# Kernel tuning notes

Hardware: AMD Instinct MI355X
Metric: run time of the kernel (lower is better)

The kernel has to match this reference:

```python
import jax, jax.numpy as jnp
import numpy as np
from jax import lax

DILATIONS = [1, 2, 4, 8, 16, 32, 64, 128, 256, 512] * 2  # 20 layers
C = 128   # residual channels
K = 2     # kernel size


def _causal_dilated_conv(x, w, b, d):
    # x: [B, C, T], w: [2C, C, K], left-pad by d*(K-1) for causality
    pad = d * (K - 1)
    y = lax.conv_general_dilated(
        x, w, window_strides=(1,), padding=[(pad, 0)],
        rhs_dilation=(d,), dimension_numbers=('NCH', 'OIH', 'NCH'))
    return y + b[None, :, None]


def setup_inputs() -> dict:
    key = jax.random.key(0)
    ks = jax.random.split(key, 5)
    L = len(DILATIONS)
    x = jax.random.normal(ks[0], (4, C, 8192), jnp.float32)
    # 0.05 scale keeps activations stable through 20 residual layers
    w_conv = jax.random.normal(ks[1], (L, 2 * C, C, K), jnp.float32) * 0.05
    b_conv = jax.random.normal(ks[2], (L, 2 * C), jnp.float32) * 0.05
    w_out = jax.random.normal(ks[3], (L, C, C), jnp.float32) * 0.05
    b_out = jax.random.normal(ks[4], (L, C), jnp.float32) * 0.05
    return {"x": x, "w_conv": w_conv, "b_conv": b_conv,
            "w_out": w_out, "b_out": b_out}


def reference(x, w_conv, b_conv, w_out, b_out):
    """WaveNet convolution stack: per layer, causal dilated conv -> gated
    tanh*sigmoid -> 1x1 output conv; residual add; collect skips.
    Returns (output [B,C,T], skips [L,B,C,T])."""
    skips = []
    for i, d in enumerate(DILATIONS):
        h = x
        z = _causal_dilated_conv(x, w_conv[i], b_conv[i], d)  # [B, 2C, T]
        g = jnp.tanh(z[:, :C]) * jax.nn.sigmoid(z[:, C:])      # gated, [B, C, T]
        s = jnp.einsum('oc,bct->bot', w_out[i], g) + b_out[i][None, :, None]
        x = s + h  # residual connection
        skips.append(s)
    return x, jnp.stack(skips)
```

## Files before the change

### kernel.cpp

```cpp
#include <hip/hip_runtime.h>
#include <hip/hip_bf16.h>
#include <stdint.h>

using f32x4  = __attribute__((ext_vector_type(4))) float;
using bf16x8 = __attribute__((ext_vector_type(8))) short;
using bf16x4 = __attribute__((ext_vector_type(4))) short;

#define NB   4
#define NC   128
#define NT   8192
#define TL   64
#define NLAYER 20
#define GROWB 272
#define CONVN (NLAYER * 256 * 256)
#define WOUTN (NLAYER * 128 * 128)
#define PACKB ((CONVN + WOUTN + 255) / 256)
#define TRANB ((NT / 64) * (NC / 64) * NB)

__device__ __forceinline__ short f2b(float f) {
  union { float f; unsigned u; } v; v.f = f;
  unsigned r = v.u + 0x7FFFu + ((v.u >> 16) & 1u);
  return (short)(r >> 16);
}

__device__ __forceinline__ float b2f(short s) {
  union { unsigned u; float f; } v;
  v.u = ((unsigned)(unsigned short)s) << 16;
  return v.f;
}

__device__ __forceinline__ f32x4 mfma16(bf16x8 a, bf16x8 b, f32x4 c) {
  return __builtin_amdgcn_mfma_f32_16x16x32_bf16(a, b, c, 0, 0, 0);
}

__device__ __forceinline__ void gl_lds16(const void* g, void* l) {
  __builtin_amdgcn_global_load_lds(
      (const __attribute__((address_space(1))) void*)g,
      (__attribute__((address_space(3))) void*)l, 16, 0, 0);
}

__global__ void prep(const float* __restrict__ x,
                     const float* __restrict__ w_conv,
                     const float* __restrict__ w_out,
                     short* __restrict__ xtb,
                     short* __restrict__ wcb, short* __restrict__ wob) {
  __shared__ float tile[64][65];
  if (blockIdx.x < PACKB) {
    const int idx = blockIdx.x * 256 + threadIdx.x;
    if (idx < CONVN) {
      const int k = idx & 255, o = (idx >> 8) & 255, lyr = idx >> 16;
      const int tap = k >> 7, c = k & 127;
      wcb[idx] = f2b(w_conv[(((size_t)lyr * 256 + o) * 128 + c) * 2 + tap]);
    } else if (idx < CONVN + WOUTN) {
      const int j = idx - CONVN;
      wob[j] = f2b(w_out[j]);
    }
    return;
  }
  const int bid2 = blockIdx.x - PACKB;
  const int t0 = (bid2 & 127) * 64;
  const int c0 = ((bid2 >> 7) & 1) * 64;
  const int b  = bid2 >> 8;
  const int lane = threadIdx.x & 63;
  const int r4   = threadIdx.x >> 6;
  #pragma unroll
  for (int i = 0; i < 16; ++i) {
    const int cl = i * 4 + r4;
    tile[cl][lane] = x[((size_t)(b * NC + c0 + cl)) * NT + t0 + lane];
  }
  __syncthreads();
  #pragma unroll
  for (int it = 0; it < 2; ++it) {
    const int idx = it * 256 + threadIdx.x;
    const int r  = idx >> 3;
    const int gi = idx & 7;
    bf16x8 v;
    #pragma unroll
    for (int jj = 0; jj < 8; ++jj) v[jj] = f2b(tile[gi * 8 + jj][r]);
    const int t = t0 + r;
    const int ci = ((c0 >> 3) + gi) ^ (t & 7);
    *(bf16x8*)((char*)xtb + ((size_t)(b * NT + t)) * 256 + ci * 16) = v;
  }
}

__global__ __launch_bounds__(512, 4)
void wavenet_pair(const short* __restrict__ wcb,
                  const float* __restrict__ b_conv,
                  const short* __restrict__ wob,
                  const float* __restrict__ b_out,
                  const short* __restrict__ xbin,
                  short* __restrict__ xbout,
                  float* __restrict__ out,
                  int L, int d1, int d2)
{
  __shared__ char ldsY[80 * 256];
  __shared__ char ldsXG[88 * 256 + 80 * 256];
  char* X = ldsXG;
  char* G = ldsXG + 88 * 256;
  char* S = ldsXG;

  const int tid = threadIdx.x;
  const int w = tid >> 6, l = tid & 63, lh = l & 15, lq = l >> 4;
  const int o0 = 16 * w + lq * 4;
  const int uid = (blockIdx.x & 7) * 64 + (blockIdx.x >> 3);
  const int b   = uid >> 7;
  const int t0  = (uid & 127) * 64;
  const bool zhalo = (t0 == 0);
  const f32x4 fz = {0.f, 0.f, 0.f, 0.f};
  const size_t XOFFS = (size_t)NB * NC * NT;

  if (!zhalo) {
    const char* src = (const char*)xbin + ((size_t)(b * NT + t0 - 24)) * 256;
    #pragma unroll
    for (int k = 0; k < 3; ++k) {
      const int off = k * 8192 + tid * 16;
      if (off < 88 * 256) gl_lds16(src + off, X + off);
    }
  } else {
    if (tid * 16 < 6144) {
      bf16x8 z = {0, 0, 0, 0, 0, 0, 0, 0};
      *(bf16x8*)(X + tid * 16) = z;
    }
    const char* src = (const char*)xbin + ((size_t)(b * NT)) * 256;
    gl_lds16(src + tid * 16,        X + 6144 + tid * 16);
    gl_lds16(src + tid * 16 + 8192, X + 6144 + tid * 16 + 8192);
  }
  __syncthreads();

  f32x4 acc1[2][5];
  #pragma unroll
  for (int mi = 0; mi < 2; ++mi)
    #pragma unroll
    for (int nn = 0; nn < 5; ++nn) acc1[mi][nn] = fz;
  {
    const short* wl = wcb + (size_t)L * 65536;
    #pragma unroll
    for (int ks = 0; ks < 8; ++ks) {
      const bf16x8 a0 = *(const bf16x8*)(wl + (16 * w + lh) * 256 + ks * 32 + lq * 8);
      const bf16x8 a1 = *(const bf16x8*)(wl + (128 + 16 * w + lh) * 256 + ks * 32 + lq * 8);
      const int dd = (ks < 4) ? d1 : 0;
      #pragma unroll
      for (int nn = 0; nn < 5; ++nn) {
        const int p = 8 + nn * 16 + lh - dd;
        const int ci = ((ks & 3) * 4 + lq) ^ (p & 7);
        const bf16x8 bb = *(const bf16x8*)(X + p * 256 + ci * 16);
        acc1[0][nn] = mfma16(a0, bb, acc1[0][nn]);
        acc1[1][nn] = mfma16(a1, bb, acc1[1][nn]);
      }
    }
  }
  {
    float ba[4], bs[4];
    #pragma unroll
    for (int r = 0; r < 4; ++r) {
      ba[r] = b_conv[L * 256 + o0 + r];
      bs[r] = b_conv[L * 256 + 128 + o0 + r];
    }
    #pragma unroll
    for (int nn = 0; nn < 5; ++nn) {
      bf16x4 g4;
      #pragma unroll
      for (int r = 0; r < 4; ++r) {
        const float za = acc1[0][nn][r] + ba[r];
        const float zb = acc1[1][nn][r] + bs[r];
        const float th = 1.f - 2.f / (1.f + __expf(2.f * za));
        const float sg = 1.f / (1.f + __expf(-zb));
        g4[r] = f2b(th * sg);
      }
      const int q = nn * 16 + lh;
      const int ci = (o0 >> 3) ^ (q & 7);
      *(bf16x4*)(G + q * 256 + ci * 16 + (o0 & 7) * 2) = g4;
    }
  }
  __syncthreads();

  f32x4 s4vL[4];
  {
    f32x4 acc2[5];
    #pragma unroll
    for (int nn = 0; nn < 5; ++nn) acc2[nn] = fz;
    const short* wol = wob + (size_t)L * 16384;
    #pragma unroll
    for (int ks = 0; ks < 4; ++ks) {
      const bf16x8 a = *(const bf16x8*)(wol + (16 * w + lh) * 128 + ks * 32 + lq * 8);
      #pragma unroll
      for (int nn = 0; nn < 5; ++nn) {
        const int q = nn * 16 + lh;
        const int ci = (ks * 4 + lq) ^ (q & 7);
        const bf16x8 bb = *(const bf16x8*)(G + q * 256 + ci * 16);
        acc2[nn] = mfma16(a, bb, acc2[nn]);
      }
    }
    float bo[4];
    #pragma unroll
    for (int r = 0; r < 4; ++r) bo[r] = b_out[L * 128 + o0 + r];
    #pragma unroll
    for (int nn = 0; nn < 5; ++nn) {
      const int q = nn * 16 + lh;
      const int p = q + 8;
      const int ci = (o0 >> 3) ^ (q & 7);
      const bf16x4 h4 = *(const bf16x4*)(X + p * 256 + ci * 16 + (o0 & 7) * 2);
      f32x4 s4, xn;
      #pragma unroll
      for (int r = 0; r < 4; ++r) {
        s4[r] = acc2[nn][r] + bo[r];
        xn[r] = s4[r] + b2f(h4[r]);
      }
      if (nn >= 1) s4vL[nn - 1] = s4;
      bf16x4 x4;
      #pragma unroll
      for (int r = 0; r < 4; ++r) x4[r] = f2b(xn[r]);
      if (zhalo && nn == 0) { x4[0] = 0; x4[1] = 0; x4[2] = 0; x4[3] = 0; }
      *(bf16x4*)(ldsY + q * 256 + ci * 16 + (o0 & 7) * 2) = x4;
    }
  }
  __syncthreads();

  #pragma unroll
  for (int nn = 0; nn < 4; ++nn) {
    const int tt = nn * 16 + lh;
    #pragma unroll
    for (int r = 0; r < 4; ++r) {
      const int o  = o0 + r;
      const int lg = tt >> 2;
      const int pg = (lg & 8) | ((lg ^ (o & 7)) & 7);
      *(float*)(S + o * 256 + pg * 16 + (tt & 3) * 4) = s4vL[nn][r];
    }
  }
  __syncthreads();

  f32x4 acc1b[2][4];
  #pragma unroll
  for (int mi = 0; mi < 2; ++mi)
    #pragma unroll
    for (int n = 0; n < 4; ++n) acc1b[mi][n] = fz;
  {
    float* skipBase = out + XOFFS + ((size_t)((L * NB + b) * NC)) * NT + t0;
    const int j8 = tid & 7;
    #pragma unroll
    for (int half = 0; half < 2; ++half) {
      const int o = half * 64 + (tid >> 3);
      #pragma unroll
      for (int k = 0; k < 2; ++k) {
        const int pg = (k * 8) | ((j8 ^ (o & 7)) & 7);
        const f32x4 v = *(const f32x4*)(S + o * 256 + pg * 16);
        __builtin_nontemporal_store(v, (f32x4*)(skipBase + (size_t)o * NT + j8 * 4 + k * 32));
      }
    }
    const short* wl2 = wcb + (size_t)(L + 1) * 65536;
    #pragma unroll
    for (int ks = 0; ks < 8; ++ks) {
      const bf16x8 a0 = *(const bf16x8*)(wl2 + (16 * w + lh) * 256 + ks * 32 + lq * 8);
      const bf16x8 a1 = *(const bf16x8*)(wl2 + (128 + 16 * w + lh) * 256 + ks * 32 + lq * 8);
      const int dd = (ks < 4) ? d2 : 0;
      #pragma unroll
      for (int n = 0; n < 4; ++n) {
        const int qy = 16 + n * 16 + lh - dd;
        const int ci = ((ks & 3) * 4 + lq) ^ (qy & 7);
        const bf16x8 bb = *(const bf16x8*)(ldsY + qy * 256 + ci * 16);
        acc1b[0][n] = mfma16(a0, bb, acc1b[0][n]);
        acc1b[1][n] = mfma16(a1, bb, acc1b[1][n]);
      }
    }
  }
  __syncthreads();

  {
    float ba[4], bs[4];
    #pragma unroll
    for (int r = 0; r < 4; ++r) {
      ba[r] = b_conv[(L + 1) * 256 + o0 + r];
      bs[r] = b_conv[(L + 1) * 256 + 128 + o0 + r];
    }
    #pragma unroll
    for (int n = 0; n < 4; ++n) {
      bf16x4 g4;
      #pragma unroll
      for (int r = 0; r < 4; ++r) {
        const float za = acc1b[0][n][r] + ba[r];
        const float zb = acc1b[1][n][r] + bs[r];
        const float th = 1.f - 2.f / (1.f + __expf(2.f * za));
        const float sg = 1.f / (1.f + __expf(-zb));
        g4[r] = f2b(th * sg);
      }
      const int q2 = n * 16 + lh;
      const int ci = (o0 >> 3) ^ (q2 & 7);
      *(bf16x4*)(G + q2 * 256 + ci * 16 + (o0 & 7) * 2) = g4;
    }
  }
  __syncthreads();

  f32x4 s4vP[4];
  {
    f32x4 acc2[4];
    #pragma unroll
    for (int n = 0; n < 4; ++n) acc2[n] = fz;
    const short* wol2 = wob + (size_t)(L + 1) * 16384;
    #pragma unroll
    for (int ks = 0; ks < 4; ++ks) {
      const bf16x8 a = *(const bf16x8*)(wol2 + (16 * w + lh) * 128 + ks * 32 + lq * 8);
      #pragma unroll
      for (int n = 0; n < 4; ++n) {
        const int q2 = n * 16 + lh;
        const int ci = (ks * 4 + lq) ^ (q2 & 7);
        const bf16x8 bb = *(const bf16x8*)(G + q2 * 256 + ci * 16);
        acc2[n] = mfma16(a, bb, acc2[n]);
      }
    }
    float bo[4];
    #pragma unroll
    for (int r = 0; r < 4; ++r) bo[r] = b_out[(L + 1) * 128 + o0 + r];
    #pragma unroll
    for (int n = 0; n < 4; ++n) {
      const int q = 16 + n * 16 + lh;
      const int ci = (o0 >> 3) ^ (q & 7);
      const bf16x4 h4 = *(const bf16x4*)(ldsY + q * 256 + ci * 16 + (o0 & 7) * 2);
      f32x4 s4, xn;
      #pragma unroll
      for (int r = 0; r < 4; ++r) {
        s4[r] = acc2[n][r] + bo[r];
        xn[r] = s4[r] + b2f(h4[r]);
      }
      s4vP[n] = s4;
      bf16x4 x4;
      #pragma unroll
      for (int r = 0; r < 4; ++r) x4[r] = f2b(xn[r]);
      *(bf16x4*)(ldsY + q * 256 + ci * 16 + (o0 & 7) * 2) = x4;
    }
  }
  __syncthreads();

  #pragma unroll
  for (int n = 0; n < 4; ++n) {
    const int tt = n * 16 + lh;
    #pragma unroll
    for (int r = 0; r < 4; ++r) {
      const int o  = o0 + r;
      const int lg = tt >> 2;
      const int pg = (lg & 8) | ((lg ^ (o & 7)) & 7);
      *(float*)(S + o * 256 + pg * 16 + (tt & 3) * 4) = s4vP[n][r];
    }
  }
  __syncthreads();

  {
    float* skipBase = out + XOFFS + ((size_t)(((L + 1) * NB + b) * NC)) * NT + t0;
    const int j8 = tid & 7;
    #pragma unroll
    for (int half = 0; half < 2; ++half) {
      const int o = half * 64 + (tid >> 3);
      #pragma unroll
      for (int k = 0; k < 2; ++k) {
        const int pg = (k * 8) | ((j8 ^ (o & 7)) & 7);
        const f32x4 v = *(const f32x4*)(S + o * 256 + pg * 16);
        __builtin_nontemporal_store(v, (f32x4*)(skipBase + (size_t)o * NT + j8 * 4 + k * 32));
      }
    }
    char* dstBase = (char*)xbout + ((size_t)(b * NT + t0)) * 256;
    #pragma unroll
    for (int k = 0; k < 2; ++k) {
      const int idx = k * 512 + tid;
      const int r = idx >> 4, pcol = idx & 15;
      *(f32x4*)(dstBase + r * 256 + pcol * 16) =
          *(const f32x4*)(ldsY + (16 + r) * 256 + pcol * 16);
    }
  }
}

__global__ __launch_bounds__(512, 4)
void wavenet_pair6(const short* __restrict__ wcb,
                   const float* __restrict__ b_conv,
                   const short* __restrict__ wob,
                   const float* __restrict__ b_out,
                   const short* __restrict__ xbin,
                   short* __restrict__ xbout,
                   float* __restrict__ out,
                   int L, int d1, int d2)
{
  __shared__ char ldsY[96 * 256];
  __shared__ char ldsXG[112 * 256 + 96 * 256];
  char* X = ldsXG;
  char* G = ldsXG + 112 * 256;
  char* S = ldsXG;

  const int tid = threadIdx.x;
  const int w = tid >> 6, l = tid & 63, lh = l & 15, lq = l >> 4;
  const int o0 = 16 * w + lq * 4;
  const int uid = (blockIdx.x & 7) * 64 + (blockIdx.x >> 3);
  const int b   = uid >> 7;
  const int t0  = (uid & 127) * 64;
  const bool zhalo = (t0 == 0);
  const f32x4 fz = {0.f, 0.f, 0.f, 0.f};
  const size_t XOFFS = (size_t)NB * NC * NT;

  if (!zhalo) {
    const char* src = (const char*)xbin + ((size_t)(b * NT + t0 - 48)) * 256;
    #pragma unroll
    for (int k = 0; k < 4; ++k) {
      const int off = k * 8192 + tid * 16;
      if (off < 112 * 256) gl_lds16(src + off, X + off);
    }
  } else {
    if (tid * 16 < 12288) {
      bf16x8 z = {0, 0, 0, 0, 0, 0, 0, 0};
      *(bf16x8*)(X + tid * 16) = z;
      if (tid * 16 + 8192 < 12288) *(bf16x8*)(X + tid * 16 + 8192) = z;
    }
    const char* src = (const char*)xbin + ((size_t)(b * NT)) * 256;
    gl_lds16(src + tid * 16,        X + 12288 + tid * 16);
    gl_lds16(src + tid * 16 + 8192, X + 12288 + tid * 16 + 8192);
  }
  __syncthreads();

  f32x4 acc1[2][6];
  #pragma unroll
  for (int mi = 0; mi < 2; ++mi)
    #pragma unroll
    for (int nn = 0; nn < 6; ++nn) acc1[mi][nn] = fz;
  {
    const short* wl = wcb + (size_t)L * 65536;
    #pragma unroll
    for (int ks = 0; ks < 8; ++ks) {
      const bf16x8 a0 = *(const bf16x8*)(wl + (16 * w + lh) * 256 + ks * 32 + lq * 8);
      const bf16x8 a1 = *(const bf16x8*)(wl + (128 + 16 * w + lh) * 256 + ks * 32 + lq * 8);
      const int dd = (ks < 4) ? d1 : 0;
      #pragma unroll
      for (int nn = 0; nn < 6; ++nn) {
        const int p = 16 + nn * 16 + lh - dd;
        const int ci = ((ks & 3) * 4 + lq) ^ (p & 7);
        const bf16x8 bb = *(const bf16x8*)(X + p * 256 + ci * 16);
        acc1[0][nn] = mfma16(a0, bb, acc1[0][nn]);
        acc1[1][nn] = mfma16(a1, bb, acc1[1][nn]);
      }
    }
  }
  {
    float ba[4], bs[4];
    #pragma unroll
    for (int r = 0; r < 4; ++r) {
      ba[r] = b_conv[L * 256 + o0 + r];
      bs[r] = b_conv[L * 256 + 128 + o0 + r];
    }
    #pragma unroll
    for (int nn = 0; nn < 6; ++nn) {
      bf16x4 g4;
      #pragma unroll
      for (int r = 0; r < 4; ++r) {
        const float za = acc1[0][nn][r] + ba[r];
        const float zb = acc1[1][nn][r] + bs[r];
        const float th = 1.f - 2.f / (1.f + __expf(2.f * za));
        const float sg = 1.f / (1.f + __expf(-zb));
        g4[r] = f2b(th * sg);
      }
      const int q = nn * 16 + lh;
      const int ci = (o0 >> 3) ^ (q & 7);
      *(bf16x4*)(G + q * 256 + ci * 16 + (o0 & 7) * 2) = g4;
    }
  }
  __syncthreads();

  f32x4 s4vL[4];
  {
    f32x4 acc2[6];
    #pragma unroll
    for (int nn = 0; nn < 6; ++nn) acc2[nn] = fz;
    const short* wol = wob + (size_t)L * 16384;
    #pragma unroll
    for (int ks = 0; ks < 4; ++ks) {
      const bf16x8 a = *(const bf16x8*)(wol + (16 * w + lh) * 128 + ks * 32 + lq * 8);
      #pragma unroll
      for (int nn = 0; nn < 6; ++nn) {
        const int q = nn * 16 + lh;
        const int ci = (ks * 4 + lq) ^ (q & 7);
        const bf16x8 bb = *(const bf16x8*)(G + q * 256 + ci * 16);
        acc2[nn] = mfma16(a, bb, acc2[nn]);
      }
    }
    float bo[4];
    #pragma unroll
    for (int r = 0; r < 4; ++r) bo[r] = b_out[L * 128 + o0 + r];
    #pragma unroll
    for (int nn = 0; nn < 6; ++nn) {
      const int q = nn * 16 + lh;
      const int p = q + 16;
      const int ci = (o0 >> 3) ^ (q & 7);
      const bf16x4 h4 = *(const bf16x4*)(X + p * 256 + ci * 16 + (o0 & 7) * 2);
      f32x4 s4, xn;
      #pragma unroll
      for (int r = 0; r < 4; ++r) {
        s4[r] = acc2[nn][r] + bo[r];
        xn[r] = s4[r] + b2f(h4[r]);
      }
      if (nn >= 2) s4vL[nn - 2] = s4;
      bf16x4 x4;
      #pragma unroll
      for (int r = 0; r < 4; ++r) x4[r] = f2b(xn[r]);
      if (zhalo && nn < 2) { x4[0] = 0; x4[1] = 0; x4[2] = 0; x4[3] = 0; }
      *(bf16x4*)(ldsY + q * 256 + ci * 16 + (o0 & 7) * 2) = x4;
    }
  }
  __syncthreads();

  #pragma unroll
  for (int nn = 0; nn < 4; ++nn) {
    const int tt = nn * 16 + lh;
    #pragma unroll
    for (int r = 0; r < 4; ++r) {
      const int o  = o0 + r;
      const int lg = tt >> 2;
      const int pg = (lg & 8) | ((lg ^ (o & 7)) & 7);
      *(float*)(S + o * 256 + pg * 16 + (tt & 3) * 4) = s4vL[nn][r];
    }
  }
  __syncthreads();

  f32x4 acc1b[2][4];
  #pragma unroll
  for (int mi = 0; mi < 2; ++mi)
    #pragma unroll
    for (int n = 0; n < 4; ++n) acc1b[mi][n] = fz;
  {
    float* skipBase = out + XOFFS + ((size_t)((L * NB + b) * NC)) * NT + t0;
    const int j8 = tid & 7;
    #pragma unroll
    for (int half = 0; half < 2; ++half) {
      const int o = half * 64 + (tid >> 3);
      #pragma unroll
      for (int k = 0; k < 2; ++k) {
        const int pg = (k * 8) | ((j8 ^ (o & 7)) & 7);
        const f32x4 v = *(const f32x4*)(S + o * 256 + pg * 16);
        __builtin_nontemporal_store(v, (f32x4*)(skipBase + (size_t)o * NT + j8 * 4 + k * 32));
      }
    }
    const short* wl2 = wcb + (size_t)(L + 1) * 65536;
    #pragma unroll
    for (int ks = 0; ks < 8; ++ks) {
      const bf16x8 a0 = *(const bf16x8*)(wl2 + (16 * w + lh) * 256 + ks * 32 + lq * 8);
      const bf16x8 a1 = *(const bf16x8*)(wl2 + (128 + 16 * w + lh) * 256 + ks * 32 + lq * 8);
      const int dd = (ks < 4) ? d2 : 0;
      #pragma unroll
      for (int n = 0; n < 4; ++n) {
        const int qy = 32 + n * 16 + lh - dd;
        const int ci = ((ks & 3) * 4 + lq) ^ (qy & 7);
        const bf16x8 bb = *(const bf16x8*)(ldsY + qy * 256 + ci * 16);
        acc1b[0][n] = mfma16(a0, bb, acc1b[0][n]);
        acc1b[1][n] = mfma16(a1, bb, acc1b[1][n]);
      }
    }
  }
  __syncthreads();

  {
    float ba[4], bs[4];
    #pragma unroll
    for (int r = 0; r < 4; ++r) {
      ba[r] = b_conv[(L + 1) * 256 + o0 + r];
      bs[r] = b_conv[(L + 1) * 256 + 128 + o0 + r];
    }
    #pragma unroll
    for (int n = 0; n < 4; ++n) {
      bf16x4 g4;
      #pragma unroll
      for (int r = 0; r < 4; ++r) {
        const float za = acc1b[0][n][r] + ba[r];
        const float zb = acc1b[1][n][r] + bs[r];
        const float th = 1.f - 2.f / (1.f + __expf(2.f * za));
        const float sg = 1.f / (1.f + __expf(-zb));
        g4[r] = f2b(th * sg);
      }
      const int q2 = n * 16 + lh;
      const int ci = (o0 >> 3) ^ (q2 & 7);
      *(bf16x4*)(G + q2 * 256 + ci * 16 + (o0 & 7) * 2) = g4;
    }
  }
  __syncthreads();

  f32x4 s4vP[4];
  {
    f32x4 acc2[4];
    #pragma unroll
    for (int n = 0; n < 4; ++n) acc2[n] = fz;
    const short* wol2 = wob + (size_t)(L + 1) * 16384;
    #pragma unroll
    for (int ks = 0; ks < 4; ++ks) {
      const bf16x8 a = *(const bf16x8*)(wol2 + (16 * w + lh) * 128 + ks * 32 + lq * 8);
      #pragma unroll
      for (int n = 0; n < 4; ++n) {
        const int q2 = n * 16 + lh;
        const int ci = (ks * 4 + lq) ^ (q2 & 7);
        const bf16x8 bb = *(const bf16x8*)(G + q2 * 256 + ci * 16);
        acc2[n] = mfma16(a, bb, acc2[n]);
      }
    }
    float bo[4];
    #pragma unroll
    for (int r = 0; r < 4; ++r) bo[r] = b_out[(L + 1) * 128 + o0 + r];
    #pragma unroll
    for (int n = 0; n < 4; ++n) {
      const int q = 32 + n * 16 + lh;
      const int ci = (o0 >> 3) ^ (q & 7);
      const bf16x4 h4 = *(const bf16x4*)(ldsY + q * 256 + ci * 16 + (o0 & 7) * 2);
      f32x4 s4, xn;
      #pragma unroll
      for (int r = 0; r < 4; ++r) {
        s4[r] = acc2[n][r] + bo[r];
        xn[r] = s4[r] + b2f(h4[r]);
      }
      s4vP[n] = s4;
      bf16x4 x4;
      #pragma unroll
      for (int r = 0; r < 4; ++r) x4[r] = f2b(xn[r]);
      *(bf16x4*)(ldsY + q * 256 + ci * 16 + (o0 & 7) * 2) = x4;
    }
  }
  __syncthreads();

  #pragma unroll
  for (int n = 0; n < 4; ++n) {
    const int tt = n * 16 + lh;
    #pragma unroll
    for (int r = 0; r < 4; ++r) {
      const int o  = o0 + r;
      const int lg = tt >> 2;
      const int pg = (lg & 8) | ((lg ^ (o & 7)) & 7);
      *(float*)(S + o * 256 + pg * 16 + (tt & 3) * 4) = s4vP[n][r];
    }
  }
  __syncthreads();

  {
    float* skipBase = out + XOFFS + ((size_t)(((L + 1) * NB + b) * NC)) * NT + t0;
    const int j8 = tid & 7;
    #pragma unroll
    for (int half = 0; half < 2; ++half) {
      const int o = half * 64 + (tid >> 3);
      #pragma unroll
      for (int k = 0; k < 2; ++k) {
        const int pg = (k * 8) | ((j8 ^ (o & 7)) & 7);
        const f32x4 v = *(const f32x4*)(S + o * 256 + pg * 16);
        __builtin_nontemporal_store(v, (f32x4*)(skipBase + (size_t)o * NT + j8 * 4 + k * 32));
      }
    }
    char* dstBase = (char*)xbout + ((size_t)(b * NT + t0)) * 256;
    #pragma unroll
    for (int k = 0; k < 2; ++k) {
      const int idx = k * 512 + tid;
      const int r = idx >> 4, pcol = idx & 15;
      *(f32x4*)(dstBase + r * 256 + pcol * 16) =
          *(const f32x4*)(ldsY + (32 + r) * 256 + pcol * 16);
    }
  }
}

__global__ __launch_bounds__(512, 4)
void wavenet_layer(const short* __restrict__ wcb,
                   const float* __restrict__ b_conv,
                   const short* __restrict__ wob,
                   const float* __restrict__ b_out,
                   const short* __restrict__ xbin,
                   short* __restrict__ xbout,
                   float* __restrict__ out,
                   int layer, int dil, int last)
{
  __shared__ char ldsXC[TL * 256];
  __shared__ char ldsSP[TL * 256 + TL * GROWB];
  char* ldsXP = ldsSP;
  char* ldsG  = ldsSP + TL * 256;
  char* ldsS  = ldsSP;

  const int tid = threadIdx.x;
  const int w   = tid >> 6;
  const int l   = tid & 63;
  const int lh  = l & 15;
  const int lq  = l >> 4;
  const int o0  = 16 * w + lq * 4;
  const int uid = (blockIdx.x & 7) * 64 + (blockIdx.x >> 3);
  const int b   = uid >> 7;
  const int t0  = (uid & 127) * 64;

  {
    const char* xcg = (const char*)xbin + ((size_t)(b * NT + t0)) * 256;
    const int off = w * 2048 + l * 16;
    gl_lds16(xcg + off, ldsXC + off);
    gl_lds16(xcg + off + 1024, ldsXC + off + 1024);
  }
  if (t0 >= dil) {
    const char* xpg = (const char*)xbin + ((size_t)(b * NT + t0 - dil)) * 256;
    const int off = w * 2048 + l * 16;
    gl_lds16(xpg + off, ldsXP + off);
    gl_lds16(xpg + off + 1024, ldsXP + off + 1024);
  } else {
    const int row = tid >> 3, j8 = tid & 7;
    const int tp = t0 + row - dil;
    char* dst = ldsXP + row * 256;
    if (tp >= 0) {
      const char* src = (const char*)xbin + ((size_t)(b * NT + tp)) * 256;
      *(bf16x8*)(dst + j8 * 16)       = *(const bf16x8*)(src + j8 * 16);
      *(bf16x8*)(dst + j8 * 16 + 128) = *(const bf16x8*)(src + j8 * 16 + 128);
    } else {
      bf16x8 z = {0, 0, 0, 0, 0, 0, 0, 0};
      *(bf16x8*)(dst + j8 * 16)       = z;
      *(bf16x8*)(dst + j8 * 16 + 128) = z;
    }
  }
  __syncthreads();

  const f32x4 fz = {0.f, 0.f, 0.f, 0.f};
  f32x4 acc1[2][4];
  #pragma unroll
  for (int mi = 0; mi < 2; ++mi)
    #pragma unroll
    for (int n = 0; n < 4; ++n) acc1[mi][n] = fz;

  const short* wl = wcb + (size_t)layer * 65536;
  #pragma unroll
  for (int ks = 0; ks < 8; ++ks) {
    const bf16x8 a0 = *(const bf16x8*)(wl + (16 * w + lh) * 256 + ks * 32 + lq * 8);
    const bf16x8 a1 = *(const bf16x8*)(wl + (128 + 16 * w + lh) * 256 + ks * 32 + lq * 8);
    const char* base = (ks < 4) ? ldsXP : ldsXC;
    const int dd = (ks < 4) ? dil : 0;
    #pragma unroll
    for (int n = 0; n < 4; ++n) {
      const int tt = n * 16 + lh;
      const int ci = ((ks & 3) * 4 + lq) ^ ((tt - dd) & 7);
      const bf16x8 bb = *(const bf16x8*)(base + tt * 256 + ci * 16);
      acc1[0][n] = mfma16(a0, bb, acc1[0][n]);
      acc1[1][n] = mfma16(a1, bb, acc1[1][n]);
    }
  }

  {
    float ba[4], bs[4];
    #pragma unroll
    for (int r = 0; r < 4; ++r) {
      ba[r] = b_conv[layer * 256 + o0 + r];
      bs[r] = b_conv[layer * 256 + 128 + o0 + r];
    }
    #pragma unroll
    for (int n = 0; n < 4; ++n) {
      bf16x4 g4;
      #pragma unroll
      for (int r = 0; r < 4; ++r) {
        const float za = acc1[0][n][r] + ba[r];
        const float zb = acc1[1][n][r] + bs[r];
        const float th = 1.f - 2.f / (1.f + __expf(2.f * za));
        const float sg = 1.f / (1.f + __expf(-zb));
        g4[r] = f2b(th * sg);
      }
      const int tt = n * 16 + lh;
      *(bf16x4*)(ldsG + tt * GROWB + o0 * 2) = g4;
    }
  }
  __syncthreads();

  f32x4 acc2[4];
  #pragma unroll
  for (int n = 0; n < 4; ++n) acc2[n] = fz;
  const short* wol = wob + (size_t)layer * 16384;
  #pragma unroll
  for (int ks = 0; ks < 4; ++ks) {
    const bf16x8 a = *(const bf16x8*)(wol + (16 * w + lh) * 128 + ks * 32 + lq * 8);
    #pragma unroll
    for (int n = 0; n < 4; ++n) {
      const int tt = n * 16 + lh;
      const bf16x8 bb = *(const bf16x8*)(ldsG + tt * GROWB + ks * 64 + lq * 16);
      acc2[n] = mfma16(a, bb, acc2[n]);
    }
  }
  __syncthreads();

  f32x4 xn4[4];
  {
    float bo[4];
    #pragma unroll
    for (int r = 0; r < 4; ++r) bo[r] = b_out[layer * 128 + o0 + r];
    #pragma unroll
    for (int n = 0; n < 4; ++n) {
      const int tt = n * 16 + lh;
      const int ci = (o0 >> 3) ^ (tt & 7);
      const bf16x4 h4 = *(const bf16x4*)(ldsXC + tt * 256 + ci * 16 + (o0 & 7) * 2);
      f32x4 s4, xn;
      #pragma unroll
      for (int r = 0; r < 4; ++r) {
        s4[r] = acc2[n][r] + bo[r];
        xn[r] = s4[r] + b2f(h4[r]);
      }
      #pragma unroll
      for (int r = 0; r < 4; ++r) {
        const int o  = o0 + r;
        const int lg = tt >> 2;
        const int pg = (lg & 8) | ((lg ^ (o & 7)) & 7);
        *(float*)(ldsS + o * 256 + pg * 16 + (tt & 3) * 4) = s4[r];
      }
      if (!last) {
        bf16x4 x4;
        #pragma unroll
        for (int r = 0; r < 4; ++r) x4[r] = f2b(xn[r]);
        *(bf16x4*)(ldsXC + tt * 256 + ci * 16 + (o0 & 7) * 2) = x4;
      } else {
        xn4[n] = xn;
      }
    }
  }
  __syncthreads();

  const size_t XOFFS = (size_t)NB * NC * NT;
  {
    float* skipBase = out + XOFFS + ((size_t)((layer * NB + b) * NC)) * NT + t0;
    const int j8 = tid & 7;
    #pragma unroll
    for (int half = 0; half < 2; ++half) {
      const int o = half * 64 + (tid >> 3);
      #pragma unroll
      for (int k = 0; k < 2; ++k) {
        const int pg = (k * 8) | ((j8 ^ (o & 7)) & 7);
        const f32x4 v = *(const f32x4*)(ldsS + o * 256 + pg * 16);
        __builtin_nontemporal_store(v, (f32x4*)(skipBase + (size_t)o * NT + j8 * 4 + k * 32));
      }
    }
  }
  if (!last) {
    char* dstBase = (char*)xbout + ((size_t)(b * NT + t0)) * 256;
    #pragma unroll
    for (int k = 0; k < 2; ++k) {
      const int idx = k * 512 + tid;
      const int r = idx >> 4, p = idx & 15;
      *(f32x4*)(dstBase + r * 256 + p * 16) = *(const f32x4*)(ldsXC + r * 256 + p * 16);
    }
  } else {
    {
      #pragma unroll
      for (int n = 0; n < 4; ++n) {
        const int tt = n * 16 + lh;
        #pragma unroll
        for (int r = 0; r < 4; ++r)
          *(short*)(ldsXC + (o0 + r) * 128 + tt * 2) = f2b(xn4[n][r]);
      }
    }
    __syncthreads();
    float* xBase = out + ((size_t)(b * NC)) * NT + t0;
    const int j16 = tid & 15;
    #pragma unroll
    for (int k = 0; k < 4; ++k) {
      const int o = k * 32 + (tid >> 4);
      const bf16x4 v = *(const bf16x4*)(ldsXC + o * 128 + j16 * 8);
      f32x4 f;
      #pragma unroll
      for (int r = 0; r < 4; ++r) f[r] = b2f(v[r]);
      __builtin_nontemporal_store(f, (f32x4*)(xBase + (size_t)o * NT + j16 * 4));
    }
  }
}

extern "C" void kernel_launch(void* const* d_in, const int* in_sizes, int n_in,
                              void* d_out, int out_size, void* d_ws, size_t ws_size,
                              hipStream_t stream) {
  const float* x      = (const float*)d_in[0];
  const float* w_conv = (const float*)d_in[1];
  const float* b_conv = (const float*)d_in[2];
  const float* w_out  = (const float*)d_in[3];
  const float* b_out  = (const float*)d_in[4];
  float* out = (float*)d_out;

  const size_t XTN = (size_t)NB * NT * NC;
  short* xb[2];
  xb[0] = (short*)d_ws;
  xb[1] = xb[0] + XTN;
  short* wcb = xb[1] + XTN;
  short* wob = wcb + CONVN;

  prep<<<dim3(PACKB + TRANB), 256, 0, stream>>>(x, w_conv, w_out, xb[0], wcb, wob);

  int cur = 0;
  wavenet_pair<<<dim3(512), 512, 0, stream>>>(wcb, b_conv, wob, b_out,
                                              xb[cur], xb[cur ^ 1], out, 0, 1, 2);
  cur ^= 1;
  wavenet_pair<<<dim3(512), 512, 0, stream>>>(wcb, b_conv, wob, b_out,
                                              xb[cur], xb[cur ^ 1], out, 2, 4, 8);
  cur ^= 1;
  wavenet_pair6<<<dim3(512), 512, 0, stream>>>(wcb, b_conv, wob, b_out,
                                               xb[cur], xb[cur ^ 1], out, 4, 16, 32);
  cur ^= 1;
  for (int i = 6; i <= 9; ++i) {
    wavenet_layer<<<dim3(512), 512, 0, stream>>>(
        wcb, b_conv, wob, b_out, xb[cur], xb[cur ^ 1], out, i, 1 << i, 0);
    cur ^= 1;
  }
  wavenet_pair<<<dim3(512), 512, 0, stream>>>(wcb, b_conv, wob, b_out,
                                              xb[cur], xb[cur ^ 1], out, 10, 1, 2);
  cur ^= 1;
  wavenet_pair<<<dim3(512), 512, 0, stream>>>(wcb, b_conv, wob, b_out,
                                              xb[cur], xb[cur ^ 1], out, 12, 4, 8);
  cur ^= 1;
  wavenet_pair6<<<dim3(512), 512, 0, stream>>>(wcb, b_conv, wob, b_out,
                                               xb[cur], xb[cur ^ 1], out, 14, 16, 32);
  cur ^= 1;
  for (int i = 16; i <= 19; ++i) {
    wavenet_layer<<<dim3(512), 512, 0, stream>>>(
        wcb, b_conv, wob, b_out, xb[cur], xb[cur ^ 1], out, i, 1 << (i - 10),
        (i == 19) ? 1 : 0);
    cur ^= 1;
  }
}
```

Before: 344.2 us.

## Replace per-layer kernel launches with a persistent cooperative kernel using flag-based sync

Adds a persistent cooperative kernel in which each of 512 blocks owns a 64-step time tile for all 20 layers. Blocks wait on per-tile flags from the producing neighbour at the right dilation offset, and on acks before overwriting a ping-pong buffer. The current x tile stays in LDS across layers. This removes the multiple kernel launches and the full-tensor reread of x per layer. The cost is spin-wait synchronization and serialized dependency chains, especially at small dilations where each tile depends on its left neighbour. The old multi-kernel path is kept as a fallback if the cooperative launch fails.

```diff
diff --git a/kernel.cpp b/kernel.cpp
--- a/kernel.cpp
+++ b/kernel.cpp
@@ -16,6 +16,7 @@
 #define WOUTN (NLAYER * 128 * 128)
 #define PACKB ((CONVN + WOUTN + 255) / 256)
 #define TRANB ((NT / 64) * (NC / 64) * NB)
+#define FLAGN (NLAYER * NB * 128)
 
 __device__ __forceinline__ short f2b(float f) {
   union { float f; unsigned u; } v; v.f = f;
@@ -80,6 +81,224 @@
     const int t = t0 + r;
     const int ci = ((c0 >> 3) + gi) ^ (t & 7);
     *(bf16x8*)((char*)xtb + ((size_t)(b * NT + t)) * 256 + ci * 16) = v;
+  }
+}
+
+__global__ __launch_bounds__(512, 4)
+void wavenet_persist(const short* __restrict__ wcb,
+                     const float* __restrict__ b_conv,
+                     const short* __restrict__ wob,
+                     const float* __restrict__ b_out,
+                     short* __restrict__ xb0,
+                     short* __restrict__ xb1,
+                     float* __restrict__ out,
+                     int* __restrict__ flags,
+                     int* __restrict__ acks)
+{
+  __shared__ char ldsXC[TL * 256];
+  __shared__ char ldsXP[TL * 256];
+  __shared__ char ldsG[TL * GROWB];
+
+  const int tid = threadIdx.x;
+  const int w   = tid >> 6;
+  const int l   = tid & 63;
+  const int lh  = l & 15;
+  const int lq  = l >> 4;
+  const int o0  = 16 * w + lq * 4;
+  const int uid = (blockIdx.x & 7) * 64 + (blockIdx.x >> 3);
+  const int b   = uid >> 7;
+  const int j   = uid & 127;
+  const int t0  = j * 64;
+  const f32x4 fz = {0.f, 0.f, 0.f, 0.f};
+  const size_t XOFFS = (size_t)NB * NC * NT;
+
+  {
+    const char* xcg = (const char*)xb0 + ((size_t)(b * NT + t0)) * 256;
+    const int off = w * 2048 + l * 16;
+    gl_lds16(xcg + off, ldsXC + off);
+    gl_lds16(xcg + off + 1024, ldsXC + off + 1024);
+  }
+
+  int dprev = 0;
+  for (int i = 0; i < NLAYER; ++i) {
+    const int d = 1 << (i < 10 ? i : i - 10);
+    const short* xbin  = (i & 1) ? xb1 : xb0;
+    short*       xbout = (i & 1) ? xb0 : xb1;
+
+    if (i > 0) {
+      int jx = -1;
+      if (d < 64) { if (j > 0) jx = j - 1; }
+      else        { if (j >= (d >> 6)) jx = j - (d >> 6); }
+      if (tid == 0 && jx >= 0) {
+        int* fp = &flags[((i - 1) * NB + b) * 128 + jx];
+        while (__hip_atomic_fetch_add(fp, 0, __ATOMIC_RELAXED,
+                                      __HIP_MEMORY_SCOPE_AGENT) == 0)
+          __builtin_amdgcn_s_sleep(8);
+        __builtin_amdgcn_fence(__ATOMIC_ACQUIRE, "agent");
+      }
+      __syncthreads();
+    }
+
+    if (t0 >= d) {
+      const char* xpg = (const char*)xbin + ((size_t)(b * NT + t0 - d)) * 256;
+      const int off = w * 2048 + l * 16;
+      gl_lds16(xpg + off, ldsXP + off);
+      gl_lds16(xpg + off + 1024, ldsXP + off + 1024);
+    } else {
+      const int row = tid >> 3, j8 = tid & 7;
+      const int tp = t0 + row - d;
+      char* dst = ldsXP + row * 256;
+      if (tp >= 0) {
+        const char* src = (const char*)xbin + ((size_t)(b * NT + tp)) * 256;
+        *(bf16x8*)(dst + j8 * 16)       = *(const bf16x8*)(src + j8 * 16);
+        *(bf16x8*)(dst + j8 * 16 + 128) = *(const bf16x8*)(src + j8 * 16 + 128);
+      } else {
+        bf16x8 z = {0, 0, 0, 0, 0, 0, 0, 0};
+        *(bf16x8*)(dst + j8 * 16)       = z;
+        *(bf16x8*)(dst + j8 * 16 + 128) = z;
+      }
+    }
+    __syncthreads();
+    if (tid == 0)
+      __hip_atomic_store(&acks[(i * NB + b) * 128 + j], 1,
+                         __ATOMIC_RELAXED, __HIP_MEMORY_SCOPE_AGENT);
+
+    f32x4 acc1[2][4];
+    #pragma unroll
+    for (int mi = 0; mi < 2; ++mi)
+      #pragma unroll
+      for (int n = 0; n < 4; ++n) acc1[mi][n] = fz;
+    const short* wl = wcb + (size_t)i * 65536;
+    #pragma unroll
+    for (int ks = 0; ks < 8; ++ks) {
+      const bf16x8 a0 = *(const bf16x8*)(wl + (16 * w + lh) * 256 + ks * 32 + lq * 8);
+      const bf16x8 a1 = *(const bf16x8*)(wl + (128 + 16 * w + lh) * 256 + ks * 32 + lq * 8);
+      const char* base = (ks < 4) ? ldsXP : ldsXC;
+      const int dd = (ks < 4) ? d : 0;
+      #pragma unroll
+      for (int n = 0; n < 4; ++n) {
+        const int tt = n * 16 + lh;
+        const int ci = ((ks & 3) * 4 + lq) ^ ((tt - dd) & 7);
+        const bf16x8 bb = *(const bf16x8*)(base + tt * 256 + ci * 16);
+        acc1[0][n] = mfma16(a0, bb, acc1[0][n]);
+        acc1[1][n] = mfma16(a1, bb, acc1[1][n]);
+      }
+    }
+
+    {
+      float ba[4], bs[4];
+      #pragma unroll
+      for (int r = 0; r < 4; ++r) {
+        ba[r] = b_conv[i * 256 + o0 + r];
+        bs[r] = b_conv[i * 256 + 128 + o0 + r];
+      }
+      #pragma unroll
+      for (int n = 0; n < 4; ++n) {
+        bf16x4 g4;
+        #pragma unroll
+        for (int r = 0; r < 4; ++r) {
+          const float za = acc1[0][n][r] + ba[r];
+          const float zb = acc1[1][n][r] + bs[r];
+          const float th = 1.f - 2.f / (1.f + __expf(2.f * za));
+          const float sg = 1.f / (1.f + __expf(-zb));
+          g4[r] = f2b(th * sg);
+        }
+        const int tt = n * 16 + lh;
+        *(bf16x4*)(ldsG + tt * GROWB + o0 * 2) = g4;
+      }
+    }
+    __syncthreads();
+
+    f32x4 acc2[4];
+    #pragma unroll
+    for (int n = 0; n < 4; ++n) acc2[n] = fz;
+    const short* wol = wob + (size_t)i * 16384;
+    #pragma unroll
+    for (int ks = 0; ks < 4; ++ks) {
+      const bf16x8 a = *(const bf16x8*)(wol + (16 * w + lh) * 128 + ks * 32 + lq * 8);
+      #pragma unroll
+      for (int n = 0; n < 4; ++n) {
+        const int tt = n * 16 + lh;
+        const bf16x8 bb = *(const bf16x8*)(ldsG + tt * GROWB + ks * 64 + lq * 16);
+        acc2[n] = mfma16(a, bb, acc2[n]);
+      }
+    }
+
+    f32x4 xn4[4];
+    {
+      float bo[4];
+      #pragma unroll
+      for (int r = 0; r < 4; ++r) bo[r] = b_out[i * 128 + o0 + r];
+      float* skipBase = out + XOFFS + ((size_t)((i * NB + b) * NC)) * NT + t0;
+      #pragma unroll
+      for (int n = 0; n < 4; ++n) {
+        const int tt = n * 16 + lh;
+        const int ci = (o0 >> 3) ^ (tt & 7);
+        const bf16x4 h4 = *(const bf16x4*)(ldsXC + tt * 256 + ci * 16 + (o0 & 7) * 2);
+        f32x4 s4, xn;
+        #pragma unroll
+        for (int r = 0; r < 4; ++r) {
+          s4[r] = acc2[n][r] + bo[r];
+          xn[r] = s4[r] + b2f(h4[r]);
+          __builtin_nontemporal_store(s4[r], skipBase + (size_t)(o0 + r) * NT + tt);
+        }
+        if (i < NLAYER - 1) {
+          bf16x4 x4;
+          #pragma unroll
+          for (int r = 0; r < 4; ++r) x4[r] = f2b(xn[r]);
+          *(bf16x4*)(ldsXC + tt * 256 + ci * 16 + (o0 & 7) * 2) = x4;
+        } else {
+          xn4[n] = xn;
+        }
+      }
+    }
+    __syncthreads();
+
+    if (i < NLAYER - 1) {
+      if (i >= 1) {
+        const int de = (dprev < 64) ? 1 : (dprev >> 6);
+        const int jr = j + de;
+        if (tid == 0 && jr < 128) {
+          int* ap = &acks[((i - 1) * NB + b) * 128 + jr];
+          while (__hip_atomic_fetch_add(ap, 0, __ATOMIC_RELAXED,
+                                        __HIP_MEMORY_SCOPE_AGENT) == 0)
+            __builtin_amdgcn_s_sleep(8);
+        }
+        __syncthreads();
+      }
+      char* dstBase = (char*)xbout + ((size_t)(b * NT + t0)) * 256;
+      #pragma unroll
+      for (int k = 0; k < 2; ++k) {
+        const int idx = k * 512 + tid;
+        const int r = idx >> 4, p = idx & 15;
+        *(f32x4*)(dstBase + r * 256 + p * 16) = *(const f32x4*)(ldsXC + r * 256 + p * 16);
+      }
+      __syncthreads();
+      if (tid == 0)
+        __hip_atomic_store(&flags[(i * NB + b) * 128 + j], 1,
+                           __ATOMIC_RELEASE, __HIP_MEMORY_SCOPE_AGENT);
+    } else {
+      #pragma unroll
+      for (int n = 0; n < 4; ++n) {
+        const int tt = n * 16 + lh;
+        #pragma unroll
+        for (int r = 0; r < 4; ++r)
+          *(short*)(ldsXC + (o0 + r) * 128 + tt * 2) = f2b(xn4[n][r]);
+      }
+      __syncthreads();
+      float* xBase = out + ((size_t)(b * NC)) * NT + t0;
+      const int j16 = tid & 15;
+      #pragma unroll
+      for (int k = 0; k < 4; ++k) {
+        const int o = k * 32 + (tid >> 4);
+        const bf16x4 v = *(const bf16x4*)(ldsXC + o * 128 + j16 * 8);
+        f32x4 f;
+        #pragma unroll
+        for (int r = 0; r < 4; ++r) f[r] = b2f(v[r]);
+        __builtin_nontemporal_store(f, (f32x4*)(xBase + (size_t)o * NT + j16 * 4));
+      }
+    }
+    dprev = d;
   }
 }
 
@@ -868,8 +1087,20 @@
   xb[1] = xb[0] + XTN;
   short* wcb = xb[1] + XTN;
   short* wob = wcb + CONVN;
-
+  int*   flags = (int*)(wob + WOUTN);
+  int*   acks  = flags + FLAGN;
+
+  hipMemsetAsync(flags, 0, 2 * FLAGN * sizeof(int), stream);
   prep<<<dim3(PACKB + TRANB), 256, 0, stream>>>(x, w_conv, w_out, xb[0], wcb, wob);
+
+  short* xb0 = xb[0];
+  short* xb1 = xb[1];
+  void* args[] = {(void*)&wcb, (void*)&b_conv, (void*)&wob, (void*)&b_out,
+                  (void*)&xb0, (void*)&xb1, (void*)&out,
+                  (void*)&flags, (void*)&acks};
+  hipError_t e = hipLaunchCooperativeKernel((void*)wavenet_persist, dim3(512),
+                                            dim3(512), args, 0, stream);
+  if (e == hipSuccess) return;
 
   int cur = 0;
   wavenet_pair<<<dim3(512), 512, 0, stream>>>(wcb, b_conv, wob, b_out,
```

New measurement: 670.9 us. 94.9% more time.
